# Optimization experiments

Hardware: AMD Instinct MI355X
Metric: run time of the kernel (lower is better)

The kernel has to match this reference:

```python
import jax, jax.numpy as jnp
import numpy as np

EPS = 1e-08


def setup_inputs() -> dict:
    key = jax.random.key(0)
    ks = jax.random.split(key, 9)
    B, T, H, W = 128, 32, 32, 32
    Z = 128
    d = {}
    d['x_seq'] = jax.random.normal(ks[0], (B, T, H, W), dtype=jnp.float32)
    # encoder MLP: 1024 -> 256 -> 128 (kaiming-ish scale)
    d['We1'] = jax.random.normal(ks[1], (H * W, 256), dtype=jnp.float32) * (2.0 / (H * W)) ** 0.5
    d['be1'] = jnp.zeros((256,), jnp.float32)
    d['We2'] = jax.random.normal(ks[2], (256, Z), dtype=jnp.float32) * (2.0 / 256) ** 0.5
    d['be2'] = jnp.zeros((Z,), jnp.float32)
    # context norm params
    d['gamma'] = jnp.ones((Z,), jnp.float32)
    d['beta'] = jnp.zeros((Z,), jnp.float32)
    # g_theta: (128+1)*2=258 -> 512 -> 256
    d['Wg1'] = jax.random.normal(ks[3], (258, 512), dtype=jnp.float32) * (2.0 / 258) ** 0.5
    d['bg1'] = jnp.zeros((512,), jnp.float32)
    d['Wg2'] = jax.random.normal(ks[4], (512, 256), dtype=jnp.float32) * (2.0 / 512) ** 0.5
    d['bg2'] = jnp.zeros((256,), jnp.float32)
    # f_phi: 256 -> 256 -> y_dim=4
    d['Wf'] = jax.random.normal(ks[5], (256, 256), dtype=jnp.float32) * (2.0 / 256) ** 0.5
    d['bf'] = jnp.zeros((256,), jnp.float32)
    d['Wy'] = jax.random.normal(ks[6], (256, 4), dtype=jnp.float32) * (1.0 / 256) ** 0.5
    d['by'] = jnp.zeros((4,), jnp.float32)
    return d


def reference(x_seq, We1, be1, We2, be2, gamma, beta, Wg1, bg1, Wg2, bg2, Wf, bf, Wy, by):
    B, T, H, W = x_seq.shape
    # Encoder (MLP stand-in), vectorized over the sequence dim
    x = x_seq.reshape(B, T, H * W)
    h = jax.nn.relu(jnp.einsum('btd,dk->btk', x, We1) + be1)
    z = jnp.einsum('btk,kz->btz', h, We2) + be2          # [B,T,128]
    # Context norm over the sequence dim (torch .var() is unbiased, ddof=1)
    mu = z.mean(axis=1, keepdims=True)
    sigma = jnp.sqrt(z.var(axis=1, keepdims=True, ddof=1) + EPS)
    z = (z - mu) / sigma * gamma + beta
    # Append temporal tag
    tag = jnp.broadcast_to(jnp.arange(T, dtype=z.dtype)[None, :, None], (B, T, 1))
    z = jnp.concatenate([z, tag], axis=2)                # [B,T,129]
    # Relation network over all T^2 ordered pairs, batched as one GEMM.
    # g_hidden = relu([z_i, z_j] @ Wg1 + bg1); split Wg1 to avoid materializing the concat.
    Wg1_a, Wg1_b = Wg1[:129], Wg1[129:]
    gi = jnp.einsum('bic,ch->bih', z, Wg1_a)             # [B,T,512]
    gj = jnp.einsum('bjc,ch->bjh', z, Wg1_b)             # [B,T,512]
    g_hidden = jax.nn.relu(gi[:, :, None, :] + gj[:, None, :, :] + bg1)  # [B,T,T,512]
    g_out = jax.nn.relu(jnp.einsum('bijh,hg->bijg', g_hidden, Wg2) + bg2)
    all_g = g_out.sum(axis=(1, 2))                       # [B,256]
    f_hidden = jax.nn.relu(all_g @ Wf + bf)
    y_pred_linear = f_hidden @ Wy + by                   # [B,4]
    y_pred = jnp.argmax(y_pred_linear, axis=1)
    return (y_pred_linear, y_pred)
```

## Files before the change

kernel.cpp:

```cpp
#include <hip/hip_runtime.h>
#include <hip/hip_bf16.h>

#define EPS 1e-8f

typedef __attribute__((ext_vector_type(8))) short short8;
typedef __attribute__((ext_vector_type(4))) float f32x4;

__device__ __forceinline__ unsigned short f2bf(float f) {
  union { float f; unsigned u; } v; v.f = f;
  unsigned r = v.u + 0x7fffu + ((v.u >> 16) & 1u);
  return (unsigned short)(r >> 16);
}
__device__ __forceinline__ float bf2f(unsigned short b) {
  union { unsigned u; float f; } v; v.u = ((unsigned)b) << 16;
  return v.f;
}
__device__ __forceinline__ unsigned pack_bf2(float lo, float hi) {
  unsigned r;
  asm("v_cvt_pk_bf16_f32 %0, %1, %2" : "=v"(r) : "v"(lo), "v"(hi));
  return r;
}

__global__ __launch_bounds__(256) void k0_prep(const float* __restrict__ We1,
                                               const float* __restrict__ We2,
                                               const float* __restrict__ Wg1,
                                               const float* __restrict__ Wg2,
                                               const float* __restrict__ Wf,
                                               unsigned short* __restrict__ We1T,
                                               unsigned short* __restrict__ We2T,
                                               unsigned short* __restrict__ Wg1T,
                                               unsigned short* __restrict__ Wg2T,
                                               unsigned short* __restrict__ WfT) {
  int idx = blockIdx.x * 256 + threadIdx.x;
  if (idx < 262144) {
    int n = idx >> 10, k = idx & 1023;
    We1T[idx] = f2bf(We1[k * 256 + n]);
  } else if (idx < 294912) {
    int e = idx - 262144;
    int n = e >> 8, k = e & 255;
    We2T[e] = f2bf(We2[k * 128 + n]);
  } else if (idx < 458752) {
    int e = idx - 294912;
    int n = e / 160, c = e % 160;
    float v = 0.f;
    if (c < 129) v = (n < 512) ? Wg1[c * 512 + n] : Wg1[(129 + c) * 512 + (n - 512)];
    Wg1T[e] = f2bf(v);
  } else if (idx < 589824) {
    int e = idx - 458752;
    int n = e >> 9, k = e & 511;
    Wg2T[e] = f2bf(Wg2[k * 256 + n]);
  } else {
    int e = idx - 589824;
    int n = e >> 8, k = e & 255;
    WfT[e] = f2bf(Wf[k * 256 + n]);
  }
}

__global__ __launch_bounds__(512, 2) void k1(const float* __restrict__ x,
                                             const unsigned short* __restrict__ We1T,
                                             const float* __restrict__ be1,
                                             unsigned short* __restrict__ h_bf) {
  __shared__ unsigned char As[2][8192];
  int tid = threadIdx.x, lane = tid & 63, w = tid >> 6;
  int m0 = blockIdx.x * 16;
  int srow = tid >> 5, skk = (tid & 31) * 8;
  int cb = w * 32;
  int row = lane & 15, kg = (lane >> 4) * 8;

  f32x4 acc[2] = {{0,0,0,0},{0,0,0,0}};

  auto stage = [&](int kc, int buf) {
    const float* src = x + (size_t)(m0 + srow) * 1024 + kc * 256 + skk;
    float4 a = *reinterpret_cast<const float4*>(src);
    float4 b = *reinterpret_cast<const float4*>(src + 4);
    uint4 pv;
    pv.x = pack_bf2(a.x, a.y); pv.y = pack_bf2(a.z, a.w);
    pv.z = pack_bf2(b.x, b.y); pv.w = pack_bf2(b.z, b.w);
    int addr = (srow * 512 + skk * 2) ^ ((srow & 7) << 4);
    *reinterpret_cast<uint4*>(&As[buf][addr]) = pv;
  };

  stage(0, 0);
  __syncthreads();
  for (int kc = 0; kc < 4; ++kc) {
    if (kc < 3) stage(kc + 1, (kc + 1) & 1);
    short8 breg[2][8];
#pragma unroll
    for (int cf = 0; cf < 2; ++cf)
#pragma unroll
      for (int ks = 0; ks < 8; ++ks)
        breg[cf][ks] = *reinterpret_cast<const short8*>(
            We1T + (size_t)(cb + cf * 16 + row) * 1024 + kc * 256 + ks * 32 + kg);
    const unsigned char* hc = &As[kc & 1][0];
#pragma unroll
    for (int ks = 0; ks < 8; ++ks) {
      int aoff = (row * 512 + ks * 64 + kg * 2) ^ ((row & 7) << 4);
      short8 af = *reinterpret_cast<const short8*>(hc + aoff);
      acc[0] = __builtin_amdgcn_mfma_f32_16x16x32_bf16(af, breg[0][ks], acc[0], 0, 0, 0);
      acc[1] = __builtin_amdgcn_mfma_f32_16x16x32_bf16(af, breg[1][ks], acc[1], 0, 0, 0);
    }
    __syncthreads();
  }
#pragma unroll
  for (int cf = 0; cf < 2; ++cf) {
    int col = cb + cf * 16 + row;
    float bias = be1[col];
#pragma unroll
    for (int r = 0; r < 4; ++r) {
      int orow = m0 + (lane >> 4) * 4 + r;
      h_bf[(size_t)orow * 256 + col] = f2bf(fmaxf(acc[cf][r] + bias, 0.f));
    }
  }
}

__global__ __launch_bounds__(256) void k2(const unsigned short* __restrict__ h_bf,
                                          const unsigned short* __restrict__ We2T,
                                          const float* __restrict__ be2,
                                          const float* __restrict__ gamma,
                                          const float* __restrict__ beta,
                                          const unsigned short* __restrict__ Wg1T,
                                          const float* __restrict__ bg1,
                                          unsigned short* __restrict__ g_all) {
  __shared__ unsigned char zcs[16384];
  __shared__ float zb[32][132];
  int b = blockIdx.x >> 2, nq = blockIdx.x & 3;
  int tid = threadIdx.x, lane = tid & 63, w = tid >> 6;
  int row = lane & 15, kg = (lane >> 4) * 8;

  {
    int srow = tid >> 3, skk = (tid & 7) * 32;
#pragma unroll
    for (int q = 0; q < 4; ++q) {
      short8 v = *reinterpret_cast<const short8*>(
          h_bf + (size_t)(b * 32 + srow) * 256 + skk + q * 8);
      int addr = (srow * 512 + (skk + q * 8) * 2) ^ ((srow & 7) << 4);
      *reinterpret_cast<short8*>(&zcs[addr]) = v;
    }
  }
  short8 breg1[2][8];
#pragma unroll
  for (int cf = 0; cf < 2; ++cf)
#pragma unroll
    for (int ks = 0; ks < 8; ++ks)
      breg1[cf][ks] = *reinterpret_cast<const short8*>(
          We2T + (size_t)(w * 32 + cf * 16 + row) * 256 + ks * 32 + kg);
  __syncthreads();

  {
    f32x4 acc[2][2] = {{{0,0,0,0},{0,0,0,0}},{{0,0,0,0},{0,0,0,0}}};
#pragma unroll
    for (int ks = 0; ks < 8; ++ks) {
      int a0off = (row * 512 + ks * 64 + kg * 2) ^ ((row & 7) << 4);
      int a1off = ((16 + row) * 512 + ks * 64 + kg * 2) ^ ((row & 7) << 4);
      short8 a0 = *reinterpret_cast<const short8*>(&zcs[a0off]);
      short8 a1 = *reinterpret_cast<const short8*>(&zcs[a1off]);
#pragma unroll
      for (int cf = 0; cf < 2; ++cf) {
        acc[0][cf] = __builtin_amdgcn_mfma_f32_16x16x32_bf16(a0, breg1[cf][ks], acc[0][cf], 0, 0, 0);
        acc[1][cf] = __builtin_amdgcn_mfma_f32_16x16x32_bf16(a1, breg1[cf][ks], acc[1][cf], 0, 0, 0);
      }
    }
#pragma unroll
    for (int rf = 0; rf < 2; ++rf)
#pragma unroll
      for (int cf = 0; cf < 2; ++cf) {
        int col = w * 32 + cf * 16 + row;
        float bias = be2[col];
#pragma unroll
        for (int r = 0; r < 4; ++r)
          zb[rf * 16 + (lane >> 4) * 4 + r][col] = acc[rf][cf][r] + bias;
      }
  }
  __syncthreads();

  if (tid < 128) {
    float s = 0.f, s2 = 0.f;
#pragma unroll 4
    for (int t = 0; t < 32; ++t) { float v = zb[t][tid]; s += v; s2 += v * v; }
    float mu = s * (1.f / 32.f);
    float var = (s2 - 32.f * mu * mu) * (1.f / 31.f);
    float rs = 1.f / sqrtf(fmaxf(var, 0.f) + EPS);
    float g = gamma[tid], be = beta[tid];
#pragma unroll 4
    for (int t = 0; t < 32; ++t) {
      unsigned short v = f2bf((zb[t][tid] - mu) * rs * g + be);
      int addr = (t * 512 + tid * 2) ^ ((t & 7) << 4);
      *reinterpret_cast<unsigned short*>(&zcs[addr]) = v;
    }
  } else if (tid < 160) {
    for (int t = 0; t < 32; ++t) {
      unsigned short v = (tid == 128) ? f2bf((float)t) : 0;
      int addr = (t * 512 + tid * 2) ^ ((t & 7) << 4);
      *reinterpret_cast<unsigned short*>(&zcs[addr]) = v;
    }
  }
  __syncthreads();

  {
    int n0 = nq * 256 + w * 64;
    short8 af[2][5];
#pragma unroll
    for (int rf = 0; rf < 2; ++rf)
#pragma unroll
      for (int ks = 0; ks < 5; ++ks) {
        int aoff = ((rf * 16 + row) * 512 + ks * 64 + kg * 2) ^ ((row & 7) << 4);
        af[rf][ks] = *reinterpret_cast<const short8*>(&zcs[aoff]);
      }
    short8 breg[4][5];
#pragma unroll
    for (int cf = 0; cf < 4; ++cf)
#pragma unroll
      for (int ks = 0; ks < 5; ++ks)
        breg[cf][ks] = *reinterpret_cast<const short8*>(
            Wg1T + (size_t)(n0 + cf * 16 + row) * 160 + ks * 32 + kg);
    f32x4 acc[2][4] = {{{0,0,0,0},{0,0,0,0},{0,0,0,0},{0,0,0,0}},
                       {{0,0,0,0},{0,0,0,0},{0,0,0,0},{0,0,0,0}}};
#pragma unroll
    for (int ks = 0; ks < 5; ++ks)
#pragma unroll
      for (int cf = 0; cf < 4; ++cf) {
        acc[0][cf] = __builtin_amdgcn_mfma_f32_16x16x32_bf16(af[0][ks], breg[cf][ks], acc[0][cf], 0, 0, 0);
        acc[1][cf] = __builtin_amdgcn_mfma_f32_16x16x32_bf16(af[1][ks], breg[cf][ks], acc[1][cf], 0, 0, 0);
      }
#pragma unroll
    for (int cf = 0; cf < 4; ++cf) {
      int n = n0 + cf * 16 + row;
      float bias = (n < 512) ? bg1[n] : 0.f;
#pragma unroll
      for (int rf = 0; rf < 2; ++rf)
#pragma unroll
        for (int r = 0; r < 4; ++r) {
          int t = rf * 16 + (lane >> 4) * 4 + r;
          g_all[((size_t)(b * 32 + t) << 10) + n] = f2bf(acc[rf][cf][r] + bias);
        }
    }
  }
}

__global__ __launch_bounds__(512, 2) void k3(const unsigned short* __restrict__ g_all,
                                             const unsigned short* __restrict__ Wg2T,
                                             const float* __restrict__ bg2,
                                             float* __restrict__ all_gp) {
  __shared__ unsigned char ldsH[2][32768];
  int b = blockIdx.x >> 2, qi = blockIdx.x & 3;
  int ii0 = qi * 8;
  int tid = threadIdx.x, lane = tid & 63, w = tid >> 6;
  int row = lane & 15, kg = (lane >> 4) * 8;
  int cb = w * 32;
  int p = tid >> 4, kslot = tid & 15;

  short8 breg[2][16];
#pragma unroll
  for (int cf = 0; cf < 2; ++cf)
#pragma unroll
    for (int ks = 0; ks < 16; ++ks)
      breg[cf][ks] = *reinterpret_cast<const short8*>(
          Wg2T + (size_t)(cb + cf * 16 + row) * 512 + ks * 32 + kg);

  float gjf[32];
  {
    const unsigned short* gjp = g_all + ((size_t)(b * 32 + p) << 10) + 512 + kslot * 8;
#pragma unroll
    for (int q = 0; q < 4; ++q) {
      short8 gv0 = *reinterpret_cast<const short8*>(gjp + q * 128);
#pragma unroll
      for (int e = 0; e < 8; ++e) gjf[q * 8 + e] = bf2f((unsigned short)gv0[e]);
    }
  }
  float biasv[2] = { bg2[cb + row], bg2[cb + 16 + row] };
  float accsum[2] = { 0.f, 0.f };

  short8 gv[4];
  auto hload = [&](int ii) {
    const unsigned short* gi = g_all + ((size_t)(b * 32 + ii) << 10) + kslot * 8;
#pragma unroll
    for (int q = 0; q < 4; ++q)
      gv[q] = *reinterpret_cast<const short8*>(gi + q * 128);
  };
  auto hstore = [&](int buf) {
    unsigned char* hb = &ldsH[buf][0] + p * 1024;
#pragma unroll
    for (int q = 0; q < 4; ++q) {
      uint4 pv;
      float f0 = fmaxf(bf2f((unsigned short)gv[q][0]) + gjf[q * 8 + 0], 0.f);
      float f1 = fmaxf(bf2f((unsigned short)gv[q][1]) + gjf[q * 8 + 1], 0.f);
      float f2 = fmaxf(bf2f((unsigned short)gv[q][2]) + gjf[q * 8 + 2], 0.f);
      float f3 = fmaxf(bf2f((unsigned short)gv[q][3]) + gjf[q * 8 + 3], 0.f);
      float f4 = fmaxf(bf2f((unsigned short)gv[q][4]) + gjf[q * 8 + 4], 0.f);
      float f5 = fmaxf(bf2f((unsigned short)gv[q][5]) + gjf[q * 8 + 5], 0.f);
      float f6 = fmaxf(bf2f((unsigned short)gv[q][6]) + gjf[q * 8 + 6], 0.f);
      float f7 = fmaxf(bf2f((unsigned short)gv[q][7]) + gjf[q * 8 + 7], 0.f);
      pv.x = pack_bf2(f0, f1); pv.y = pack_bf2(f2, f3);
      pv.z = pack_bf2(f4, f5); pv.w = pack_bf2(f6, f7);
      int addr = (kslot * 16 + q * 256) ^ ((p & 7) << 4);
      *reinterpret_cast<uint4*>(hb + addr) = pv;
    }
  };

  hload(ii0);
  hstore(0);
  __syncthreads();

  for (int it = 0; it < 8; ++it) {
    if (it < 7) hload(ii0 + it + 1);
    const unsigned char* hc = &ldsH[it & 1][0];
    f32x4 acc[2][2] = {{{0,0,0,0},{0,0,0,0}},{{0,0,0,0},{0,0,0,0}}};
    short8 a0 = *reinterpret_cast<const short8*>(hc + ((row * 1024 + kg * 2) ^ ((row & 7) << 4)));
    short8 a1 = *reinterpret_cast<const short8*>(hc + (((16 + row) * 1024 + kg * 2) ^ ((row & 7) << 4)));
#pragma unroll
    for (int ks = 0; ks < 16; ++ks) {
      short8 c0v = a0, c1v = a1;
      if (ks < 15) {
        a0 = *reinterpret_cast<const short8*>(hc + ((row * 1024 + (ks + 1) * 64 + kg * 2) ^ ((row & 7) << 4)));
        a1 = *reinterpret_cast<const short8*>(hc + (((16 + row) * 1024 + (ks + 1) * 64 + kg * 2) ^ ((row & 7) << 4)));
      }
      __builtin_amdgcn_s_setprio(1);
      acc[0][0] = __builtin_amdgcn_mfma_f32_16x16x32_bf16(c0v, breg[0][ks], acc[0][0], 0, 0, 0);
      acc[0][1] = __builtin_amdgcn_mfma_f32_16x16x32_bf16(c0v, breg[1][ks], acc[0][1], 0, 0, 0);
      acc[1][0] = __builtin_amdgcn_mfma_f32_16x16x32_bf16(c1v, breg[0][ks], acc[1][0], 0, 0, 0);
      acc[1][1] = __builtin_amdgcn_mfma_f32_16x16x32_bf16(c1v, breg[1][ks], acc[1][1], 0, 0, 0);
      __builtin_amdgcn_s_setprio(0);
    }
    if (it < 7) hstore((it + 1) & 1);
#pragma unroll
    for (int cf = 0; cf < 2; ++cf)
#pragma unroll
      for (int rf = 0; rf < 2; ++rf)
#pragma unroll
        for (int r = 0; r < 4; ++r)
          accsum[cf] += fmaxf(acc[rf][cf][r] + biasv[cf], 0.f);
    __syncthreads();
  }

#pragma unroll
  for (int cf = 0; cf < 2; ++cf) {
    accsum[cf] += __shfl_xor(accsum[cf], 16, 64);
    accsum[cf] += __shfl_xor(accsum[cf], 32, 64);
  }
  if ((lane >> 4) == 0) {
#pragma unroll
    for (int cf = 0; cf < 2; ++cf)
      all_gp[(size_t)(qi * 128 + b) * 256 + cb + cf * 16 + lane] = accsum[cf];
  }
}

__global__ __launch_bounds__(512) void k4(const float* __restrict__ all_gp,
                                          const unsigned short* __restrict__ WfT,
                                          const float* __restrict__ bfv,
                                          const float* __restrict__ Wy,
                                          const float* __restrict__ by,
                                          float* __restrict__ out) {
  __shared__ unsigned char As[8192];
  __shared__ float fh[16][264];
  __shared__ float wys[1024];
  __shared__ float yvs[16][4];
  int tid = threadIdx.x, lane = tid & 63, w = tid >> 6;
  int row = lane & 15, kg = (lane >> 4) * 8;
  int m0 = blockIdx.x * 16;

  {
    int r = tid >> 5, c8 = (tid & 31) * 8;
    float s[8];
#pragma unroll
    for (int e = 0; e < 8; ++e) s[e] = 0.f;
#pragma unroll
    for (int q = 0; q < 4; ++q) {
      const float* p0 = all_gp + (size_t)(q * 128 + m0 + r) * 256 + c8;
      float4 a0 = *reinterpret_cast<const float4*>(p0);
      float4 a1 = *reinterpret_cast<const float4*>(p0 + 4);
      s[0] += a0.x; s[1] += a0.y; s[2] += a0.z; s[3] += a0.w;
      s[4] += a1.x; s[5] += a1.y; s[6] += a1.z; s[7] += a1.w;
    }
    uint4 pv;
    pv.x = pack_bf2(s[0], s[1]); pv.y = pack_bf2(s[2], s[3]);
    pv.z = pack_bf2(s[4], s[5]); pv.w = pack_bf2(s[6], s[7]);
    int addr = (r * 512 + c8 * 2) ^ ((r & 7) << 4);
    *reinterpret_cast<uint4*>(&As[addr]) = pv;
  }
  wys[tid] = Wy[tid];
  wys[tid + 512] = Wy[tid + 512];
  short8 breg[2][8];
#pragma unroll
  for (int cf = 0; cf < 2; ++cf)
#pragma unroll
    for (int ks = 0; ks < 8; ++ks)
      breg[cf][ks] = *reinterpret_cast<const short8*>(
          WfT + (size_t)(w * 32 + cf * 16 + row) * 256 + ks * 32 + kg);
  __syncthreads();

  f32x4 acc[2] = {{0,0,0,0},{0,0,0,0}};
#pragma unroll
  for (int ks = 0; ks < 8; ++ks) {
    int aoff = (row * 512 + ks * 64 + kg * 2) ^ ((row & 7) << 4);
    short8 af = *reinterpret_cast<const short8*>(&As[aoff]);
    acc[0] = __builtin_amdgcn_mfma_f32_16x16x32_bf16(af, breg[0][ks], acc[0], 0, 0, 0);
    acc[1] = __builtin_amdgcn_mfma_f32_16x16x32_bf16(af, breg[1][ks], acc[1], 0, 0, 0);
  }
#pragma unroll
  for (int cf = 0; cf < 2; ++cf) {
    int col = w * 32 + cf * 16 + row;
    float bias = bfv[col];
#pragma unroll
    for (int r = 0; r < 4; ++r)
      fh[(lane >> 4) * 4 + r][col] = fmaxf(acc[cf][r] + bias, 0.f);
  }
  __syncthreads();

  if (tid < 64) {
    int r = tid >> 2, o = tid & 3;
    float y = by[o];
#pragma unroll 4
    for (int k = 0; k < 256; ++k) y += fh[r][k] * wys[k * 4 + o];
    yvs[r][o] = y;
    out[(m0 + r) * 4 + o] = y;
  }
  __syncthreads();
  if (tid < 16) {
    int am = 0;
    float best = yvs[tid][0];
#pragma unroll
    for (int o = 1; o < 4; ++o)
      if (yvs[tid][o] > best) { best = yvs[tid][o]; am = o; }
    out[512 + m0 + tid] = (float)am;
  }
}

extern "C" void kernel_launch(void* const* d_in, const int* in_sizes, int n_in,
                              void* d_out, int out_size, void* d_ws, size_t ws_size,
                              hipStream_t stream) {
  const float* x     = (const float*)d_in[0];
  const float* We1   = (const float*)d_in[1];
  const float* be1   = (const float*)d_in[2];
  const float* We2   = (const float*)d_in[3];
  const float* be2   = (const float*)d_in[4];
  const float* gamma = (const float*)d_in[5];
  const float* beta  = (const float*)d_in[6];
  const float* Wg1   = (const float*)d_in[7];
  const float* bg1   = (const float*)d_in[8];
  const float* Wg2   = (const float*)d_in[9];
  const float* bg2   = (const float*)d_in[10];
  const float* Wf    = (const float*)d_in[11];
  const float* bff   = (const float*)d_in[12];
  const float* Wy    = (const float*)d_in[13];
  const float* by    = (const float*)d_in[14];

  char* ws = (char*)d_ws;
  unsigned short* h_bf  = (unsigned short*)(ws + 0);
  unsigned short* g_all = (unsigned short*)(ws + 2097152);
  unsigned short* We1T  = (unsigned short*)(ws + 10485760);
  unsigned short* We2T  = (unsigned short*)(ws + 11010048);
  unsigned short* Wg1T  = (unsigned short*)(ws + 11075584);
  unsigned short* Wg2T  = (unsigned short*)(ws + 11403264);
  float*          all_gp= (float*)(ws + 11665408);
  unsigned short* WfT   = (unsigned short*)(ws + 12189696);
  float*          out   = (float*)d_out;

  k0_prep<<<2560, 256, 0, stream>>>(We1, We2, Wg1, Wg2, Wf, We1T, We2T, Wg1T, Wg2T, WfT);
  k1<<<256, 512, 0, stream>>>(x, We1T, be1, h_bf);
  k2<<<512, 256, 0, stream>>>(h_bf, We2T, be2, gamma, beta, Wg1T, bg1, g_all);
  k3<<<512, 512, 0, stream>>>(g_all, Wg2T, bg2, all_gp);
  k4<<<8, 512, 0, stream>>>(all_gp, WfT, bff, Wy, by, out);
}
```

Baseline: 92.38 us.

## Halve k3 grid, interleave LDS staging with MFMA, keep gj in bf16 registers

```diff
diff --git a/kernel.cpp b/kernel.cpp
--- a/kernel.cpp
+++ b/kernel.cpp
@@ -242,8 +242,8 @@
                                              const float* __restrict__ bg2,
                                              float* __restrict__ all_gp) {
   __shared__ unsigned char ldsH[2][32768];
-  int b = blockIdx.x >> 2, qi = blockIdx.x & 3;
-  int ii0 = qi * 8;
+  int b = blockIdx.x >> 1, hi = blockIdx.x & 1;
+  int ii0 = hi * 16;
   int tid = threadIdx.x, lane = tid & 63, w = tid >> 6;
   int row = lane & 15, kg = (lane >> 4) * 8;
   int cb = w * 32;
@@ -257,15 +257,12 @@
       breg[cf][ks] = *reinterpret_cast<const short8*>(
           Wg2T + (size_t)(cb + cf * 16 + row) * 512 + ks * 32 + kg);
 
-  float gjf[32];
+  short8 gjr[4];
   {
     const unsigned short* gjp = g_all + ((size_t)(b * 32 + p) << 10) + 512 + kslot * 8;
 #pragma unroll
-    for (int q = 0; q < 4; ++q) {
-      short8 gv0 = *reinterpret_cast<const short8*>(gjp + q * 128);
-#pragma unroll
-      for (int e = 0; e < 8; ++e) gjf[q * 8 + e] = bf2f((unsigned short)gv0[e]);
-    }
+    for (int q = 0; q < 4; ++q)
+      gjr[q] = *reinterpret_cast<const short8*>(gjp + q * 128);
   }
   float biasv[2] = { bg2[cb + row], bg2[cb + 16 + row] };
   float accsum[2] = { 0.f, 0.f };
@@ -277,42 +274,48 @@
     for (int q = 0; q < 4; ++q)
       gv[q] = *reinterpret_cast<const short8*>(gi + q * 128);
   };
-  auto hstore = [&](int buf) {
+  auto hstore_q = [&](int buf, int q) {
     unsigned char* hb = &ldsH[buf][0] + p * 1024;
-#pragma unroll
-    for (int q = 0; q < 4; ++q) {
-      uint4 pv;
-      float f0 = fmaxf(bf2f((unsigned short)gv[q][0]) + gjf[q * 8 + 0], 0.f);
-      float f1 = fmaxf(bf2f((unsigned short)gv[q][1]) + gjf[q * 8 + 1], 0.f);
-      float f2 = fmaxf(bf2f((unsigned short)gv[q][2]) + gjf[q * 8 + 2], 0.f);
-      float f3 = fmaxf(bf2f((unsigned short)gv[q][3]) + gjf[q * 8 + 3], 0.f);
-      float f4 = fmaxf(bf2f((unsigned short)gv[q][4]) + gjf[q * 8 + 4], 0.f);
-      float f5 = fmaxf(bf2f((unsigned short)gv[q][5]) + gjf[q * 8 + 5], 0.f);
-      float f6 = fmaxf(bf2f((unsigned short)gv[q][6]) + gjf[q * 8 + 6], 0.f);
-      float f7 = fmaxf(bf2f((unsigned short)gv[q][7]) + gjf[q * 8 + 7], 0.f);
-      pv.x = pack_bf2(f0, f1); pv.y = pack_bf2(f2, f3);
-      pv.z = pack_bf2(f4, f5); pv.w = pack_bf2(f6, f7);
-      int addr = (kslot * 16 + q * 256) ^ ((p & 7) << 4);
-      *reinterpret_cast<uint4*>(hb + addr) = pv;
-    }
+    float f0 = fmaxf(bf2f((unsigned short)gv[q][0]) + bf2f((unsigned short)gjr[q][0]), 0.f);
+    float f1 = fmaxf(bf2f((unsigned short)gv[q][1]) + bf2f((unsigned short)gjr[q][1]), 0.f);
+    float f2 = fmaxf(bf2f((unsigned short)gv[q][2]) + bf2f((unsigned short)gjr[q][2]), 0.f);
+    float f3 = fmaxf(bf2f((unsigned short)gv[q][3]) + bf2f((unsigned short)gjr[q][3]), 0.f);
+    float f4 = fmaxf(bf2f((unsigned short)gv[q][4]) + bf2f((unsigned short)gjr[q][4]), 0.f);
+    float f5 = fmaxf(bf2f((unsigned short)gv[q][5]) + bf2f((unsigned short)gjr[q][5]), 0.f);
+    float f6 = fmaxf(bf2f((unsigned short)gv[q][6]) + bf2f((unsigned short)gjr[q][6]), 0.f);
+    float f7 = fmaxf(bf2f((unsigned short)gv[q][7]) + bf2f((unsigned short)gjr[q][7]), 0.f);
+    uint4 pv;
+    pv.x = pack_bf2(f0, f1); pv.y = pack_bf2(f2, f3);
+    pv.z = pack_bf2(f4, f5); pv.w = pack_bf2(f6, f7);
+    int addr = (kslot * 16 + q * 256) ^ ((p & 7) << 4);
+    *reinterpret_cast<uint4*>(hb + addr) = pv;
   };
 
   hload(ii0);
-  hstore(0);
-  __syncthreads();
-
-  for (int it = 0; it < 8; ++it) {
-    if (it < 7) hload(ii0 + it + 1);
+#pragma unroll
+  for (int q = 0; q < 4; ++q) hstore_q(0, q);
+  __syncthreads();
+
+  auto aread = [&](const unsigned char* hc, int r, int ks) {
+    return *reinterpret_cast<const short8*>(
+        hc + ((r * 1024 + ks * 64 + kg * 2) ^ ((r & 7) << 4)));
+  };
+
+  for (int it = 0; it < 16; ++it) {
+    if (it < 15) hload(ii0 + it + 1);
     const unsigned char* hc = &ldsH[it & 1][0];
+    int nbuf = (it + 1) & 1;
+    bool more = (it < 15);
     f32x4 acc[2][2] = {{{0,0,0,0},{0,0,0,0}},{{0,0,0,0},{0,0,0,0}}};
-    short8 a0 = *reinterpret_cast<const short8*>(hc + ((row * 1024 + kg * 2) ^ ((row & 7) << 4)));
-    short8 a1 = *reinterpret_cast<const short8*>(hc + (((16 + row) * 1024 + kg * 2) ^ ((row & 7) << 4)));
+    short8 ar[2][2];
+    ar[0][0] = aread(hc, row, 0);      ar[0][1] = aread(hc, 16 + row, 0);
+    ar[1][0] = aread(hc, row, 1);      ar[1][1] = aread(hc, 16 + row, 1);
 #pragma unroll
     for (int ks = 0; ks < 16; ++ks) {
-      short8 c0v = a0, c1v = a1;
-      if (ks < 15) {
-        a0 = *reinterpret_cast<const short8*>(hc + ((row * 1024 + (ks + 1) * 64 + kg * 2) ^ ((row & 7) << 4)));
-        a1 = *reinterpret_cast<const short8*>(hc + (((16 + row) * 1024 + (ks + 1) * 64 + kg * 2) ^ ((row & 7) << 4)));
+      short8 c0v = ar[ks & 1][0], c1v = ar[ks & 1][1];
+      if (ks < 14) {
+        ar[ks & 1][0] = aread(hc, row, ks + 2);
+        ar[ks & 1][1] = aread(hc, 16 + row, ks + 2);
       }
       __builtin_amdgcn_s_setprio(1);
       acc[0][0] = __builtin_amdgcn_mfma_f32_16x16x32_bf16(c0v, breg[0][ks], acc[0][0], 0, 0, 0);
@@ -320,8 +323,13 @@
       acc[1][0] = __builtin_amdgcn_mfma_f32_16x16x32_bf16(c1v, breg[0][ks], acc[1][0], 0, 0, 0);
       acc[1][1] = __builtin_amdgcn_mfma_f32_16x16x32_bf16(c1v, breg[1][ks], acc[1][1], 0, 0, 0);
       __builtin_amdgcn_s_setprio(0);
-    }
-    if (it < 7) hstore((it + 1) & 1);
+      if (more) {
+        if (ks == 3)  hstore_q(nbuf, 0);
+        if (ks == 6)  hstore_q(nbuf, 1);
+        if (ks == 9)  hstore_q(nbuf, 2);
+        if (ks == 12) hstore_q(nbuf, 3);
+      }
+    }
 #pragma unroll
     for (int cf = 0; cf < 2; ++cf)
 #pragma unroll
@@ -340,7 +348,7 @@
   if ((lane >> 4) == 0) {
 #pragma unroll
     for (int cf = 0; cf < 2; ++cf)
-      all_gp[(size_t)(qi * 128 + b) * 256 + cb + cf * 16 + lane] = accsum[cf];
+      all_gp[(size_t)(hi * 128 + b) * 256 + cb + cf * 16 + lane] = accsum[cf];
   }
 }
 
@@ -364,7 +372,7 @@
 #pragma unroll
     for (int e = 0; e < 8; ++e) s[e] = 0.f;
 #pragma unroll
-    for (int q = 0; q < 4; ++q) {
+    for (int q = 0; q < 2; ++q) {
       const float* p0 = all_gp + (size_t)(q * 128 + m0 + r) * 256 + c8;
       float4 a0 = *reinterpret_cast<const float4*>(p0);
       float4 a1 = *reinterpret_cast<const float4*>(p0 + 4);
@@ -452,12 +460,12 @@
   unsigned short* Wg1T  = (unsigned short*)(ws + 11075584);
   unsigned short* Wg2T  = (unsigned short*)(ws + 11403264);
   float*          all_gp= (float*)(ws + 11665408);
-  unsigned short* WfT   = (unsigned short*)(ws + 12189696);
+  unsigned short* WfT   = (unsigned short*)(ws + 11927552);
   float*          out   = (float*)d_out;
 
   k0_prep<<<2560, 256, 0, stream>>>(We1, We2, Wg1, Wg2, Wf, We1T, We2T, Wg1T, Wg2T, WfT);
   k1<<<256, 512, 0, stream>>>(x, We1T, be1, h_bf);
   k2<<<512, 256, 0, stream>>>(h_bf, We2T, be2, gamma, beta, Wg1T, bg1, g_all);
-  k3<<<512, 512, 0, stream>>>(g_all, Wg2T, bg2, all_gp);
+  k3<<<256, 512, 0, stream>>>(g_all, Wg2T, bg2, all_gp);
   k4<<<8, 512, 0, stream>>>(all_gp, WfT, bff, Wy, by, out);
 }
```

Result: slower. 105.0 us (+13.6%).
